# Performance work log

Measured on AMD Instinct MI355X. Metric: run time of the kernel, lower is better.

The kernel has to match this reference:

```python
import jax, jax.numpy as jnp
import numpy as np

B, N, D, H = 2, 512, 128, 8
DK = D // H

def setup_inputs() -> dict:
    key = jax.random.key(0)
    ks = jax.random.split(key, 7)
    s = lambda fan_in: 1.0 / np.sqrt(fan_in)
    return {
        "n": jax.random.normal(ks[0], (B, N, D), dtype=jnp.float32),
        "e": jax.random.normal(ks[1], (B, N, N, D), dtype=jnp.float32),
        "W_qkv": jax.random.normal(ks[2], (D, 3 * D), dtype=jnp.float32) * s(D),
        "O_n": jax.random.normal(ks[3], (D, D), dtype=jnp.float32) * s(D),
        "W_g": jax.random.normal(ks[4], (D, H), dtype=jnp.float32) * s(D),
        "W_e": jax.random.normal(ks[5], (D, H), dtype=jnp.float32) * s(D),
        "O_e": jax.random.normal(ks[6], (H, D), dtype=jnp.float32) * s(H),
    }

def reference(n, e, W_qkv, O_n, W_g, W_e, O_e):
    b, nn_, d = n.shape
    # QKV projection -> [B, H, N, DK] each
    qkv = (n @ W_qkv).reshape(b, nn_, 3, H, DK)
    qkv = jnp.transpose(qkv, (2, 0, 3, 1, 4))
    Q, K, V = qkv[0], qkv[1], qkv[2]
    # Edge bias and gate: [B, H, N, N]
    E = jnp.einsum('bnmd,dh->bhnm', e, W_e)
    G = jax.nn.sigmoid(jnp.einsum('bnmd,dh->bhnm', e, W_g))
    dyn_cent = jnp.log1p(G.sum(-1))  # [B, H, N]
    # Attention scores with clamp + edge bias
    A_raw = jnp.einsum('bhnd,bhmd->bhnm', Q, K) * (DK ** -0.5)
    A_raw = jnp.clip(A_raw, -5.0, 5.0)
    _E = A_raw + E
    A = jax.nn.softmax(_E, axis=-1)
    # Weighted values, rescaled by dynamic centrality
    _V = jnp.einsum('bhnm,bhmd->bhnd', A, V) * dyn_cent[..., None]
    n_out = jnp.transpose(_V, (0, 2, 1, 3)).reshape(b, nn_, d) @ O_n
    e_out = jnp.einsum('bhnm,hd->bnmd', _E, O_e)
    return n_out, e_out
```

## Files before the change

kernel.cpp:

```cpp
#include <hip/hip_runtime.h>
#include <math.h>

#define BB 2
#define NN 512
#define DD 128
#define HH 8
#define DKK 16
#define TR 128
#define NT (NN / TR)
#define ETS 516

typedef __attribute__((ext_vector_type(8))) short short8;
typedef __attribute__((ext_vector_type(4))) float f32x4;

__device__ __forceinline__ float dot4(float4 a, float4 b) {
    return a.x*b.x + a.y*b.y + a.z*b.z + a.w*b.w;
}
__device__ __forceinline__ unsigned pk_bf16(float a, float b) {
    unsigned ua = __float_as_uint(a), ub = __float_as_uint(b);
    ua = (ua + 0x7FFFu + ((ua >> 16) & 1u)) >> 16;
    ub = (ub + 0x7FFFu + ((ub >> 16) & 1u)) >> 16;
    return ua | (ub << 16);
}

__global__ __launch_bounds__(128)
void qkv_kernel(const float* __restrict__ n_in,
                const float* __restrict__ W_qkv,
                const float* __restrict__ W_g,
                const float* __restrict__ W_e,
                float* __restrict__ Qw, float* __restrict__ Kw,
                float* __restrict__ Vw, float* __restrict__ WegT)
{
    const int bid = blockIdx.x;
    if (bid >= BB * NN) {
        const int col = bid - BB * NN;
        const int t = threadIdx.x;
        WegT[col * DD + t] = (col < 8) ? W_e[t * HH + col]
                                       : W_g[t * HH + (col - 8)];
        return;
    }
    __shared__ float nrow[DD];
    const int bn = bid;
    const int b  = bn >> 9;
    const int nr = bn & 511;
    const int t  = threadIdx.x;
    nrow[t] = n_in[(size_t)bn * DD + t];
    __syncthreads();
    const int h = t >> 4, dk = t & 15;
    const size_t dst = ((size_t)(b * HH + h) * NN + nr) * DKK + dk;
    float accq = 0.f, acck = 0.f, accv = 0.f;
    #pragma unroll 8
    for (int d = 0; d < DD; ++d) {
        const float nv = nrow[d];
        const float* wr = W_qkv + (size_t)d * 3 * DD;
        accq += nv * wr[t];
        acck += nv * wr[t + 128];
        accv += nv * wr[t + 256];
    }
    Qw[dst] = accq;
    Kw[dst] = acck;
    Vw[dst] = accv;
}

__global__ __attribute__((amdgpu_flat_work_group_size(512, 512),
                          amdgpu_waves_per_eu(2, 4)))
void eg_kernel(const float* __restrict__ e,
               const float* __restrict__ WegT,
               const float* __restrict__ O_e,
               const float* __restrict__ Qw,
               const float* __restrict__ Kw,
               const float* __restrict__ Vw,
               const float* __restrict__ O_n,
               float* __restrict__ n_out,
               float* __restrict__ e_out)
{
    __shared__ __align__(16) uint4 ebuf4[TR * 16];
    __shared__ __align__(16) float ET[HH * ETS];
    __shared__ float Gred[64];
    __shared__ float dc[HH];
    __shared__ __align__(16) float vout[DD];

    const int t    = threadIdx.x;
    const int bn   = blockIdx.x;
    const int b    = bn >> 9;
    const int nr   = bn & 511;
    const int wq   = t >> 6;
    const int lane = t & 63;
    const int c    = lane & 15;
    const int mq   = lane >> 4;
    const int c4o  = t & 31;
    const int mr0  = t >> 5;

    const float4* __restrict__ e4    = (const float4*)e + (size_t)bn * NN * 32;
    const float4* __restrict__ WegT4 = (const float4*)WegT;

    short8 wB[4];
    #pragma unroll
    for (int kb = 0; kb < 4; ++kb) {
        const float4 wa = WegT4[c * 32 + kb * 8 + mq * 2];
        const float4 wb = WegT4[c * 32 + kb * 8 + mq * 2 + 1];
        uint4 u;
        u.x = pk_bf16(wa.x, wa.y); u.y = pk_bf16(wa.z, wa.w);
        u.z = pk_bf16(wb.x, wb.y); u.w = pk_bf16(wb.z, wb.w);
        wB[kb] = *(short8*)&u;
    }

    float4 pa0, pa1, pa2, pa3, pb0, pb1, pb2, pb3;

    #define STAGE_LOAD(tile)                                                  \
    {                                                                         \
        const float4* __restrict__ sp = e4 + (size_t)(tile) * 4096 + 2 * t;   \
        pa0 = sp[0];    pb0 = sp[1];                                          \
        pa1 = sp[1024]; pb1 = sp[1025];                                       \
        pa2 = sp[2048]; pb2 = sp[2049];                                       \
        pa3 = sp[3072]; pb3 = sp[3073];                                       \
    }
    #define STAGE_WRITE(P, A, B)                                              \
    {                                                                         \
        const int ms = (P) * 32 + (t >> 4), ck = t & 15;                      \
        uint4 u;                                                              \
        u.x = pk_bf16(A.x, A.y); u.y = pk_bf16(A.z, A.w);                     \
        u.z = pk_bf16(B.x, B.y); u.w = pk_bf16(B.z, B.w);                     \
        ebuf4[ms * 16 + (ck ^ (ms & 15))] = u;                                \
    }
    #define STAGE_WRITE_ALL()                                                 \
    {                                                                         \
        STAGE_WRITE(0, pa0, pb0); STAGE_WRITE(1, pa1, pb1);                   \
        STAGE_WRITE(2, pa2, pb2); STAGE_WRITE(3, pa3, pb3);                   \
    }

    float ga0 = 0.f, ga1 = 0.f, ga2 = 0.f, ga3 = 0.f;

    STAGE_LOAD(0);

    {
        const int h = wq;
        const float4* __restrict__ qp =
            (const float4*)(Qw + ((size_t)(b * HH + h) * NN + nr) * DKK);
        const float4 q0 = qp[0], q1 = qp[1], q2 = qp[2], q3 = qp[3];
        const float4* __restrict__ kb =
            (const float4*)(Kw + ((size_t)(b * HH + h) * NN) * DKK);
        #pragma unroll
        for (int k = 0; k < 8; ++k) {
            const int m = k * 64 + lane;
            float s = dot4(q0, kb[m * 4 + 0]) + dot4(q1, kb[m * 4 + 1])
                    + dot4(q2, kb[m * 4 + 2]) + dot4(q3, kb[m * 4 + 3]);
            s *= 0.25f;
            ET[h * ETS + m] = fminf(5.f, fmaxf(-5.f, s));
        }
    }

    STAGE_WRITE_ALL();
    asm volatile("s_waitcnt lgkmcnt(0)" ::: "memory");
    __builtin_amdgcn_s_barrier();

    #pragma unroll
    for (int tt = 0; tt < NT; ++tt) {
        if (tt + 1 < NT) STAGE_LOAD(tt + 1);

        const int mrow = wq * 16 + c;
        f32x4 acc = {0.f, 0.f, 0.f, 0.f};
        #pragma unroll
        for (int kb = 0; kb < 4; ++kb) {
            const int ck = kb * 4 + mq;
            uint4 av = ebuf4[mrow * 16 + (ck ^ (mrow & 15))];
            acc = __builtin_amdgcn_mfma_f32_16x16x32_bf16(
                      *(short8*)&av, wB[kb], acc, 0, 0, 0);
        }

        const int mloc = tt * TR + wq * 16 + mq * 4;
        if (c < 8) {
            float4 prev = *(float4*)&ET[c * ETS + mloc];
            prev.x += acc[0]; prev.y += acc[1];
            prev.z += acc[2]; prev.w += acc[3];
            *(float4*)&ET[c * ETS + mloc] = prev;
        } else {
            ga0 += 1.f / (1.f + __expf(-acc[0]));
            ga1 += 1.f / (1.f + __expf(-acc[1]));
            ga2 += 1.f / (1.f + __expf(-acc[2]));
            ga3 += 1.f / (1.f + __expf(-acc[3]));
        }
        asm volatile("s_waitcnt lgkmcnt(0)" ::: "memory");
        __builtin_amdgcn_s_barrier();

        if (tt + 1 < NT) {
            STAGE_WRITE_ALL();
            asm volatile("s_waitcnt lgkmcnt(0)" ::: "memory");
            __builtin_amdgcn_s_barrier();
        }
    }

    if (c >= 8) {
        float s = ga0 + ga1 + ga2 + ga3;
        s += __shfl_xor(s, 16, 64);
        s += __shfl_xor(s, 32, 64);
        if (lane < 16) Gred[wq * 8 + (c - 8)] = s;
    }
    __syncthreads();
    if (t < 8) {
        float s = 0.f;
        #pragma unroll
        for (int w = 0; w < 8; ++w) s += Gred[w * 8 + t];
        dc[t] = log1pf(s);
    }
    __syncthreads();

    {
        float4 oe[8];
        #pragma unroll
        for (int h = 0; h < 8; ++h)
            oe[h] = ((const float4*)O_e)[h * 32 + c4o];
        float4* __restrict__ out4 = (float4*)e_out + (size_t)bn * NN * 32;
        #pragma unroll 4
        for (int it = 0; it < 32; ++it) {
            const int m = mr0 + it * 16;
            float4 rr{0.f, 0.f, 0.f, 0.f};
            #pragma unroll
            for (int h = 0; h < 8; ++h) {
                const float ev = ET[h * ETS + m];
                rr.x += ev * oe[h].x;
                rr.y += ev * oe[h].y;
                rr.z += ev * oe[h].z;
                rr.w += ev * oe[h].w;
            }
            out4[m * 32 + c4o] = rr;
        }
    }

    {
        const int h = wq;
        float vals[8];
        float rmax = -1e30f;
        #pragma unroll
        for (int k = 0; k < 8; ++k) {
            vals[k] = ET[h * ETS + k * 64 + lane];
            rmax = fmaxf(rmax, vals[k]);
        }
        #pragma unroll
        for (int off = 32; off >= 1; off >>= 1)
            rmax = fmaxf(rmax, __shfl_xor(rmax, off, 64));
        float sum = 0.f;
        #pragma unroll
        for (int k = 0; k < 8; ++k) sum += __expf(vals[k] - rmax);
        #pragma unroll
        for (int off = 32; off >= 1; off >>= 1)
            sum += __shfl_xor(sum, off, 64);
        const float factor = dc[h] / sum;

        const int ddx = lane & 15, mg = lane >> 4;
        const float* __restrict__ vb = Vw + ((size_t)(b * HH + h) * NN) * DKK;
        float av = 0.f;
        #pragma unroll 4
        for (int m = mg; m < NN; m += 4) {
            const float p = __expf(ET[h * ETS + m] - rmax);
            av += p * vb[m * DKK + ddx];
        }
        av += __shfl_xor(av, 16, 64);
        av += __shfl_xor(av, 32, 64);
        if (mg == 0) vout[h * DKK + ddx] = av * factor;
    }
    __syncthreads();

    if (t < DD) {
        float a3 = 0.f;
        #pragma unroll 4
        for (int d = 0; d < DD; ++d) a3 += vout[d] * O_n[d * DD + t];
        n_out[(size_t)bn * DD + t] = a3;
    }
    #undef STAGE_LOAD
    #undef STAGE_WRITE
    #undef STAGE_WRITE_ALL
}

extern "C" void kernel_launch(void* const* d_in, const int* in_sizes, int n_in,
                              void* d_out, int out_size, void* d_ws, size_t ws_size,
                              hipStream_t stream)
{
    const float* n_ptr = (const float*)d_in[0];
    const float* e     = (const float*)d_in[1];
    const float* W_qkv = (const float*)d_in[2];
    const float* O_n   = (const float*)d_in[3];
    const float* W_g   = (const float*)d_in[4];
    const float* W_e   = (const float*)d_in[5];
    const float* O_e   = (const float*)d_in[6];

    float* n_out = (float*)d_out;
    float* e_out = n_out + (size_t)BB * NN * DD;

    float* Qw   = (float*)d_ws;
    float* Kw   = Qw + (size_t)BB * HH * NN * DKK;
    float* Vw   = Kw + (size_t)BB * HH * NN * DKK;
    float* WegT = Vw + (size_t)BB * HH * NN * DKK;

    qkv_kernel<<<BB * NN + 16, 128, 0, stream>>>(n_ptr, W_qkv, W_g, W_e,
                                                 Qw, Kw, Vw, WegT);
    eg_kernel<<<BB * NN, 512, 0, stream>>>(e, WegT, O_e, Qw, Kw, Vw, O_n,
                                           n_out, e_out);
}
```

Measured before the change: 156.0 us.

## Halve edge tile size and alternate wave halves per tile to cut registers

Shrinks the staged edge tile from 128 to 64 rows so each thread holds half as many prefetch registers, and changes launch bounds to allow more waves per CU. With 64-row tiles only four waves' worth of MFMA work exists per tile, so the two halves of the block alternate tiles, each computing on every other one. The aim is higher occupancy to hide global-load latency on the large edge tensor. The cost is twice as many barrier-separated iterations and half the waves idle during each compute step.

```diff
diff --git a/kernel.cpp b/kernel.cpp
--- a/kernel.cpp
+++ b/kernel.cpp
@@ -6,7 +6,7 @@
 #define DD 128
 #define HH 8
 #define DKK 16
-#define TR 128
+#define TR 64
 #define NT (NN / TR)
 #define ETS 516
 
@@ -62,8 +62,7 @@
     Vw[dst] = accv;
 }
 
-__global__ __attribute__((amdgpu_flat_work_group_size(512, 512),
-                          amdgpu_waves_per_eu(2, 4)))
+__global__ __launch_bounds__(512, 8)
 void eg_kernel(const float* __restrict__ e,
                const float* __restrict__ WegT,
                const float* __restrict__ O_e,
@@ -88,6 +87,8 @@
     const int lane = t & 63;
     const int c    = lane & 15;
     const int mq   = lane >> 4;
+    const int wgrp = wq & 3;
+    const int wpar = wq >> 2;
     const int c4o  = t & 31;
     const int mr0  = t >> 5;
 
@@ -105,28 +106,25 @@
         wB[kb] = *(short8*)&u;
     }
 
-    float4 pa0, pa1, pa2, pa3, pb0, pb1, pb2, pb3;
+    float4 pa0, pb0, pa1, pb1;
 
     #define STAGE_LOAD(tile)                                                  \
     {                                                                         \
-        const float4* __restrict__ sp = e4 + (size_t)(tile) * 4096 + 2 * t;   \
+        const float4* __restrict__ sp = e4 + (size_t)(tile) * 2048 + 2 * t;   \
         pa0 = sp[0];    pb0 = sp[1];                                          \
         pa1 = sp[1024]; pb1 = sp[1025];                                       \
-        pa2 = sp[2048]; pb2 = sp[2049];                                       \
-        pa3 = sp[3072]; pb3 = sp[3073];                                       \
-    }
-    #define STAGE_WRITE(P, A, B)                                              \
+    }
+    #define STAGE_WRITE(U, A, B)                                              \
     {                                                                         \
-        const int ms = (P) * 32 + (t >> 4), ck = t & 15;                      \
-        uint4 u;                                                              \
-        u.x = pk_bf16(A.x, A.y); u.y = pk_bf16(A.z, A.w);                     \
-        u.z = pk_bf16(B.x, B.y); u.w = pk_bf16(B.z, B.w);                     \
-        ebuf4[ms * 16 + (ck ^ (ms & 15))] = u;                                \
+        const int u_ = (U), ms = u_ >> 4, ck = u_ & 15;                       \
+        uint4 x;                                                              \
+        x.x = pk_bf16(A.x, A.y); x.y = pk_bf16(A.z, A.w);                     \
+        x.z = pk_bf16(B.x, B.y); x.w = pk_bf16(B.z, B.w);                     \
+        ebuf4[ms * 16 + (ck ^ (ms & 15))] = x;                                \
     }
     #define STAGE_WRITE_ALL()                                                 \
     {                                                                         \
-        STAGE_WRITE(0, pa0, pb0); STAGE_WRITE(1, pa1, pb1);                   \
-        STAGE_WRITE(2, pa2, pb2); STAGE_WRITE(3, pa3, pb3);                   \
+        STAGE_WRITE(t, pa0, pb0); STAGE_WRITE(t + 512, pa1, pb1);             \
     }
 
     float ga0 = 0.f, ga1 = 0.f, ga2 = 0.f, ga3 = 0.f;
@@ -158,27 +156,28 @@
     for (int tt = 0; tt < NT; ++tt) {
         if (tt + 1 < NT) STAGE_LOAD(tt + 1);
 
-        const int mrow = wq * 16 + c;
-        f32x4 acc = {0.f, 0.f, 0.f, 0.f};
-        #pragma unroll
-        for (int kb = 0; kb < 4; ++kb) {
-            const int ck = kb * 4 + mq;
-            uint4 av = ebuf4[mrow * 16 + (ck ^ (mrow & 15))];
-            acc = __builtin_amdgcn_mfma_f32_16x16x32_bf16(
-                      *(short8*)&av, wB[kb], acc, 0, 0, 0);
-        }
-
-        const int mloc = tt * TR + wq * 16 + mq * 4;
-        if (c < 8) {
-            float4 prev = *(float4*)&ET[c * ETS + mloc];
-            prev.x += acc[0]; prev.y += acc[1];
-            prev.z += acc[2]; prev.w += acc[3];
-            *(float4*)&ET[c * ETS + mloc] = prev;
-        } else {
-            ga0 += 1.f / (1.f + __expf(-acc[0]));
-            ga1 += 1.f / (1.f + __expf(-acc[1]));
-            ga2 += 1.f / (1.f + __expf(-acc[2]));
-            ga3 += 1.f / (1.f + __expf(-acc[3]));
+        if (wpar == (tt & 1)) {
+            const int mrow = wgrp * 16 + c;
+            f32x4 acc = {0.f, 0.f, 0.f, 0.f};
+            #pragma unroll
+            for (int kb = 0; kb < 4; ++kb) {
+                const int ck = kb * 4 + mq;
+                uint4 av = ebuf4[mrow * 16 + (ck ^ (mrow & 15))];
+                acc = __builtin_amdgcn_mfma_f32_16x16x32_bf16(
+                          *(short8*)&av, wB[kb], acc, 0, 0, 0);
+            }
+            const int mloc = tt * TR + wgrp * 16 + mq * 4;
+            if (c < 8) {
+                float4 prev = *(float4*)&ET[c * ETS + mloc];
+                prev.x += acc[0]; prev.y += acc[1];
+                prev.z += acc[2]; prev.w += acc[3];
+                *(float4*)&ET[c * ETS + mloc] = prev;
+            } else {
+                ga0 += 1.f / (1.f + __expf(-acc[0]));
+                ga1 += 1.f / (1.f + __expf(-acc[1]));
+                ga2 += 1.f / (1.f + __expf(-acc[2]));
+                ga3 += 1.f / (1.f + __expf(-acc[3]));
+            }
         }
         asm volatile("s_waitcnt lgkmcnt(0)" ::: "memory");
         __builtin_amdgcn_s_barrier();
```

Measured after the change: 370.9 us. 138% more time.

## Load edge tiles directly into MFMA operand registers, dropping LDS staging

Applied to the files above, without the earlier changes.

Removes the shared-memory staging buffer for the edge tensor, along with its double-buffered prefetch and the per-tile barriers. Each lane now reads its MFMA A-operand fragment straight from global memory and converts it to bf16 in registers, and each wave handles four 16-row groups with no block-level synchronisation. This cuts LDS traffic, LDS footprint and barrier stalls. The cost is less coalesced global loads, since each lane fetches two adjacent float4s from strided rows, and the explicit prefetch that overlapped loads with compute is gone.

```diff
diff --git a/kernel.cpp b/kernel.cpp
--- a/kernel.cpp
+++ b/kernel.cpp
@@ -6,8 +6,6 @@
 #define DD 128
 #define HH 8
 #define DKK 16
-#define TR 128
-#define NT (NN / TR)
 #define ETS 516
 
 typedef __attribute__((ext_vector_type(8))) short short8;
@@ -74,7 +72,6 @@
                float* __restrict__ n_out,
                float* __restrict__ e_out)
 {
-    __shared__ __align__(16) uint4 ebuf4[TR * 16];
     __shared__ __align__(16) float ET[HH * ETS];
     __shared__ float Gred[64];
     __shared__ float dc[HH];
@@ -105,34 +102,6 @@
         wB[kb] = *(short8*)&u;
     }
 
-    float4 pa0, pa1, pa2, pa3, pb0, pb1, pb2, pb3;
-
-    #define STAGE_LOAD(tile)                                                  \
-    {                                                                         \
-        const float4* __restrict__ sp = e4 + (size_t)(tile) * 4096 + 2 * t;   \
-        pa0 = sp[0];    pb0 = sp[1];                                          \
-        pa1 = sp[1024]; pb1 = sp[1025];                                       \
-        pa2 = sp[2048]; pb2 = sp[2049];                                       \
-        pa3 = sp[3072]; pb3 = sp[3073];                                       \
-    }
-    #define STAGE_WRITE(P, A, B)                                              \
-    {                                                                         \
-        const int ms = (P) * 32 + (t >> 4), ck = t & 15;                      \
-        uint4 u;                                                              \
-        u.x = pk_bf16(A.x, A.y); u.y = pk_bf16(A.z, A.w);                     \
-        u.z = pk_bf16(B.x, B.y); u.w = pk_bf16(B.z, B.w);                     \
-        ebuf4[ms * 16 + (ck ^ (ms & 15))] = u;                                \
-    }
-    #define STAGE_WRITE_ALL()                                                 \
-    {                                                                         \
-        STAGE_WRITE(0, pa0, pb0); STAGE_WRITE(1, pa1, pb1);                   \
-        STAGE_WRITE(2, pa2, pb2); STAGE_WRITE(3, pa3, pb3);                   \
-    }
-
-    float ga0 = 0.f, ga1 = 0.f, ga2 = 0.f, ga3 = 0.f;
-
-    STAGE_LOAD(0);
-
     {
         const int h = wq;
         const float4* __restrict__ qp =
@@ -149,26 +118,48 @@
             ET[h * ETS + m] = fminf(5.f, fmaxf(-5.f, s));
         }
     }
-
-    STAGE_WRITE_ALL();
-    asm volatile("s_waitcnt lgkmcnt(0)" ::: "memory");
-    __builtin_amdgcn_s_barrier();
+    __syncthreads();
+
+    float ga0 = 0.f, ga1 = 0.f, ga2 = 0.f, ga3 = 0.f;
 
     #pragma unroll
-    for (int tt = 0; tt < NT; ++tt) {
-        if (tt + 1 < NT) STAGE_LOAD(tt + 1);
-
-        const int mrow = wq * 16 + c;
+    for (int j = 0; j < 4; ++j) {
+        const int g    = wq + 8 * j;
+        const int mrow = g * 16 + c;
+
+        const float4* __restrict__ ep = e4 + (size_t)mrow * 32 + mq * 2;
+        const float4 ev0 = ep[0],  ev1 = ep[1];
+        const float4 ev2 = ep[8],  ev3 = ep[9];
+        const float4 ev4 = ep[16], ev5 = ep[17];
+        const float4 ev6 = ep[24], ev7 = ep[25];
+
         f32x4 acc = {0.f, 0.f, 0.f, 0.f};
-        #pragma unroll
-        for (int kb = 0; kb < 4; ++kb) {
-            const int ck = kb * 4 + mq;
-            uint4 av = ebuf4[mrow * 16 + (ck ^ (mrow & 15))];
-            acc = __builtin_amdgcn_mfma_f32_16x16x32_bf16(
-                      *(short8*)&av, wB[kb], acc, 0, 0, 0);
-        }
-
-        const int mloc = tt * TR + wq * 16 + mq * 4;
+        {
+            uint4 u;
+            u.x = pk_bf16(ev0.x, ev0.y); u.y = pk_bf16(ev0.z, ev0.w);
+            u.z = pk_bf16(ev1.x, ev1.y); u.w = pk_bf16(ev1.z, ev1.w);
+            acc = __builtin_amdgcn_mfma_f32_16x16x32_bf16(*(short8*)&u, wB[0], acc, 0, 0, 0);
+        }
+        {
+            uint4 u;
+            u.x = pk_bf16(ev2.x, ev2.y); u.y = pk_bf16(ev2.z, ev2.w);
+            u.z = pk_bf16(ev3.x, ev3.y); u.w = pk_bf16(ev3.z, ev3.w);
+            acc = __builtin_amdgcn_mfma_f32_16x16x32_bf16(*(short8*)&u, wB[1], acc, 0, 0, 0);
+        }
+        {
+            uint4 u;
+            u.x = pk_bf16(ev4.x, ev4.y); u.y = pk_bf16(ev4.z, ev4.w);
+            u.z = pk_bf16(ev5.x, ev5.y); u.w = pk_bf16(ev5.z, ev5.w);
+            acc = __builtin_amdgcn_mfma_f32_16x16x32_bf16(*(short8*)&u, wB[2], acc, 0, 0, 0);
+        }
+        {
+            uint4 u;
+            u.x = pk_bf16(ev6.x, ev6.y); u.y = pk_bf16(ev6.z, ev6.w);
+            u.z = pk_bf16(ev7.x, ev7.y); u.w = pk_bf16(ev7.z, ev7.w);
+            acc = __builtin_amdgcn_mfma_f32_16x16x32_bf16(*(short8*)&u, wB[3], acc, 0, 0, 0);
+        }
+
+        const int mloc = g * 16 + mq * 4;
         if (c < 8) {
             float4 prev = *(float4*)&ET[c * ETS + mloc];
             prev.x += acc[0]; prev.y += acc[1];
@@ -179,14 +170,6 @@
             ga1 += 1.f / (1.f + __expf(-acc[1]));
             ga2 += 1.f / (1.f + __expf(-acc[2]));
             ga3 += 1.f / (1.f + __expf(-acc[3]));
-        }
-        asm volatile("s_waitcnt lgkmcnt(0)" ::: "memory");
-        __builtin_amdgcn_s_barrier();
-
-        if (tt + 1 < NT) {
-            STAGE_WRITE_ALL();
-            asm volatile("s_waitcnt lgkmcnt(0)" ::: "memory");
-            __builtin_amdgcn_s_barrier();
         }
     }
 
@@ -267,9 +250,6 @@
         for (int d = 0; d < DD; ++d) a3 += vout[d] * O_n[d * DD + t];
         n_out[(size_t)bn * DD + t] = a3;
     }
-    #undef STAGE_LOAD
-    #undef STAGE_WRITE
-    #undef STAGE_WRITE_ALL
 }
 
 extern "C" void kernel_launch(void* const* d_in, const int* in_sizes, int n_in,
```

Result: slower. 161.4 us (+3.5%).
